# Kernel tuning notes

Hardware: AMD Instinct MI355X
Metric: run time of the kernel (lower is better)

## Reference

```python
import jax, jax.numpy as jnp
import numpy as np

T, N, F = 96, 1140, 64   # timesteps, nodes per graph, node feature dim
H = 32                    # GAT hidden channels
LH = 250                  # LSTM hidden
OUT = 2280                # per-head output
E = 22800                 # edges per graph


def setup_inputs() -> dict:
    key = jax.random.key(0)
    ks = jax.random.split(key, 32)
    s = lambda k, shape, fan: jax.random.normal(k, shape, jnp.float32) / np.sqrt(fan)
    inp = {}
    inp["nodes"] = jax.random.normal(ks[0], (T, N, F), jnp.float32)
    inp["edges_index"] = jax.random.randint(ks[1], (T, 2, E), 0, N)
    inp["edges_attr"] = jax.random.normal(ks[2], (T, E), jnp.float32)  # unused by forward (faithful)
    # GAT layer 1 (F -> H) and layer 2 (H -> H), heads=1
    inp["gat_W1"] = s(ks[3], (F, H), F)
    inp["gat_as1"] = s(ks[4], (H,), H)
    inp["gat_ad1"] = s(ks[5], (H,), H)
    inp["gat_b1"] = jnp.zeros((H,), jnp.float32)
    inp["gat_W2"] = s(ks[6], (H, H), H)
    inp["gat_as2"] = s(ks[7], (H,), H)
    inp["gat_ad2"] = s(ks[8], (H,), H)
    inp["gat_b2"] = jnp.zeros((H,), jnp.float32)
    # 2-layer LSTM, batch_first, batch=1, input = N*H
    IN0 = N * H
    inp["Wih0"] = s(ks[9], (4 * LH, IN0), IN0)
    inp["Whh0"] = s(ks[10], (4 * LH, LH), LH)
    inp["bih0"] = jnp.zeros((4 * LH,), jnp.float32)
    inp["bhh0"] = jnp.zeros((4 * LH,), jnp.float32)
    inp["Wih1"] = s(ks[11], (4 * LH, LH), LH)
    inp["Whh1"] = s(ks[12], (4 * LH, LH), LH)
    inp["bih1"] = jnp.zeros((4 * LH,), jnp.float32)
    inp["bhh1"] = jnp.zeros((4 * LH,), jnp.float32)
    # random initial states (original uses torch.randn in forward)
    inp["h0"] = jax.random.normal(ks[13], (2, 1, LH), jnp.float32)
    inp["c0"] = jax.random.normal(ks[14], (2, 1, LH), jnp.float32)
    for i in range(4):
        inp[f"fc{i+1}_W"] = s(ks[15 + 2 * i], (OUT, LH), LH)
        inp[f"fc{i+1}_b"] = jnp.zeros((OUT,), jnp.float32)
    return inp


def _gat_conv(x, src, dst, W, a_s, a_d, b, n):
    # GATConv, heads=1: h = xW; e_ij = LeakyReLU(a_s.h_src + a_d.h_dst);
    # softmax over edges sharing a destination; scatter-add aggregation.
    h = x @ W                                                   # [N, H]
    e = jax.nn.leaky_relu((h @ a_s)[src] + (h @ a_d)[dst], negative_slope=0.2)
    m = jax.ops.segment_max(e, dst, num_segments=n)
    ex = jnp.exp(e - m[dst])
    denom = jax.ops.segment_sum(ex, dst, num_segments=n)
    alpha = ex / denom[dst]
    return jax.ops.segment_sum(alpha[:, None] * h[src], dst, num_segments=n) + b


def _lstm_layer(xs, Wih, Whh, bih, bhh, h0, c0):
    # xs: [T, B, in]; torch gate order i, f, g, o
    def step(carry, x):
        h, c = carry
        g = x @ Wih.T + h @ Whh.T + bih + bhh
        i, f, gg, o = jnp.split(g, 4, axis=-1)
        c = jax.nn.sigmoid(f) * c + jax.nn.sigmoid(i) * jnp.tanh(gg)
        h = jax.nn.sigmoid(o) * jnp.tanh(c)
        return (h, c), h
    (_, _), ys = jax.lax.scan(step, (h0, c0), xs)
    return ys


def reference(nodes, edges_index, edges_attr, gat_W1, gat_as1, gat_ad1, gat_b1,
              gat_W2, gat_as2, gat_ad2, gat_b2,
              Wih0, Whh0, bih0, bhh0, Wih1, Whh1, bih1, bhh1, h0, c0,
              fc1_W, fc1_b, fc2_W, fc2_b, fc3_W, fc3_b, fc4_W, fc4_b):
    n = nodes.shape[1]
    loop = jnp.arange(n)  # self-loops (GATConv default add_self_loops=True)

    def per_graph(x, ei):
        src = jnp.concatenate([ei[0], loop])
        dst = jnp.concatenate([ei[1], loop])
        h = jax.nn.relu(_gat_conv(x, src, dst, gat_W1, gat_as1, gat_ad1, gat_b1, n))
        h = _gat_conv(h, src, dst, gat_W2, gat_as2, gat_ad2, gat_b2, n)
        return h.reshape(-1)

    seq = jax.vmap(per_graph)(nodes, edges_index)   # [T, N*H]
    xs = seq[:, None, :]                            # [T, 1, N*H] (batch=1)
    ys = _lstm_layer(xs, Wih0, Whh0, bih0, bhh0, h0[0], c0[0])
    ys = _lstm_layer(ys, Wih1, Whh1, bih1, bhh1, h0[1], c0[1])
    last = ys[-1]                                   # [1, LH]
    preds = [last @ fc1_W.T + fc1_b, last @ fc2_W.T + fc2_b,
             last @ fc3_W.T + fc3_b, last @ fc4_W.T + fc4_b]
    return jnp.stack(preds, axis=0).reshape(last.shape[0], 4, -1)  # [1, 4, 2280]
```

## Files before the change

### kernel.cpp

```cpp
#include <hip/hip_runtime.h>

#define T_ 96
#define N_ 1140
#define F_ 64
#define H_ 32
#define E_ 22800
#define LH_ 250
#define G4_ 1000
#define OUT_ 2280
#define KIN_ 36480
#define SPLITK 60
#define KC 32
#define BN 32
#define FEATB 13680
#define CNTB 8550

typedef _Float16 h2_t __attribute__((ext_vector_type(2)));

__device__ __forceinline__ float leaky02(float x){ return x > 0.f ? x : 0.2f*x; }
__device__ __forceinline__ float fsigm(float x){ return 1.f/(1.f + __expf(-x)); }
__device__ __forceinline__ float ftanh(float x){
  x = fminf(fmaxf(x, -15.f), 15.f);
  float t = __expf(2.f * x);
  return (t - 1.f) / (t + 1.f);
}
__device__ __forceinline__ unsigned packh2(float a, float b) {
  auto p = __builtin_amdgcn_cvt_pkrtz(a, b);
  return __builtin_bit_cast(unsigned, p);
}
__device__ __forceinline__ float fdot2u(unsigned w, unsigned h, float acc) {
  return __builtin_amdgcn_fdot2(__builtin_bit_cast(h2_t, w),
                                __builtin_bit_cast(h2_t, h), acc, false);
}

__device__ __forceinline__ void st_agent_u(unsigned* p, unsigned v) {
  __hip_atomic_store(p, v, __ATOMIC_RELAXED, __HIP_MEMORY_SCOPE_AGENT);
}
__device__ __forceinline__ unsigned ld_agent_u(const unsigned* p) {
  return __hip_atomic_load((unsigned*)p, __ATOMIC_RELAXED, __HIP_MEMORY_SCOPE_AGENT);
}
__device__ __forceinline__ void st_agent_i(int* p, int v) {
  __hip_atomic_store(p, v, __ATOMIC_RELAXED, __HIP_MEMORY_SCOPE_AGENT);
}
__device__ __forceinline__ int ld_agent_i(const int* p) {
  return __hip_atomic_load((int*)p, __ATOMIC_RELAXED, __HIP_MEMORY_SCOPE_AGENT);
}

__global__ void k_featcnt(const float* __restrict__ x, const float* __restrict__ W,
                          const float* __restrict__ as_, const float* __restrict__ ad_,
                          float* __restrict__ Hout, float* __restrict__ HS,
                          float* __restrict__ HD,
                          const int* __restrict__ ei, int* __restrict__ counts) {
  int tid = threadIdx.x;
  if (blockIdx.x >= FEATB) {
    int gid = (blockIdx.x - FEATB) * 256 + tid;
    if (gid >= T_ * E_) return;
    int t = gid / E_; int k = gid - t * E_;
    int dst = ei[(size_t)t * 2 * E_ + E_ + k];
    atomicAdd(&counts[t * N_ + dst], 1);
    return;
  }
  __shared__ float Wl[F_ * H_];
  __shared__ float asl[32], adl[32];
  for (int i = tid; i < F_ * H_; i += 256) Wl[i] = W[i];
  if (tid < 32) { asl[tid] = as_[tid]; adl[tid] = ad_[tid]; }
  __syncthreads();
  int row = blockIdx.x * 8 + (tid >> 5);
  int c = tid & 31;
  const float4* xr = (const float4*)(x + (size_t)row * F_);
  float acc = 0.f;
  for (int k4 = 0; k4 < (F_ >> 2); ++k4) {
    float4 v = xr[k4];
    acc += v.x * Wl[(4 * k4 + 0) * H_ + c];
    acc += v.y * Wl[(4 * k4 + 1) * H_ + c];
    acc += v.z * Wl[(4 * k4 + 2) * H_ + c];
    acc += v.w * Wl[(4 * k4 + 3) * H_ + c];
  }
  Hout[(size_t)row * H_ + c] = acc;
  float ps = acc * asl[c], pd = acc * adl[c];
  #pragma unroll
  for (int off = 16; off > 0; off >>= 1) {
    ps += __shfl_xor(ps, off, 32);
    pd += __shfl_xor(pd, off, 32);
  }
  if (c == 0) { HS[row] = ps; HD[row] = pd; }
}

__global__ void k_scan(const int* __restrict__ counts, int* __restrict__ offs,
                       int* __restrict__ cursor) {
  int t = blockIdx.x; int tid = threadIdx.x;
  int base = tid * 5;
  int v[5]; int s = 0;
  #pragma unroll
  for (int r = 0; r < 5; ++r) {
    int i = base + r;
    int c = (i < N_) ? counts[t * N_ + i] : 0;
    v[r] = c; s += c;
  }
  __shared__ int sh[256];
  sh[tid] = s; __syncthreads();
  for (int off = 1; off < 256; off <<= 1) {
    int add = (tid >= off) ? sh[tid - off] : 0;
    __syncthreads();
    sh[tid] += add;
    __syncthreads();
  }
  int run = sh[tid] - s;
  #pragma unroll
  for (int r = 0; r < 5; ++r) {
    int i = base + r;
    if (i < N_) { offs[t * (N_ + 1) + i] = run; cursor[t * N_ + i] = run; }
    run += v[r];
  }
  if (tid == 255) offs[t * (N_ + 1) + N_] = sh[255];
}

__global__ void k_fill(const int* __restrict__ ei, int* __restrict__ cursor,
                       int* __restrict__ elist) {
  int gid = blockIdx.x * blockDim.x + threadIdx.x;
  if (gid >= T_ * E_) return;
  int t = gid / E_; int k = gid - t * E_;
  int src = ei[(size_t)t * 2 * E_ + k];
  int dst = ei[(size_t)t * 2 * E_ + E_ + k];
  int pos = atomicAdd(&cursor[t * N_ + dst], 1);
  elist[(size_t)t * E_ + pos] = src;
}

__global__ void k_aggrfeat(const float* __restrict__ Hf, const float* __restrict__ HS,
                           const float* __restrict__ HD, const int* __restrict__ offs,
                           const int* __restrict__ elist, const float* __restrict__ b,
                           const float* __restrict__ W2, const float* __restrict__ as2,
                           const float* __restrict__ ad2,
                           float* __restrict__ H2, float* __restrict__ HS2,
                           float* __restrict__ HD2) {
  __shared__ float W2l[H_ * H_];
  __shared__ float as2l[32], ad2l[32];
  int tid = threadIdx.x;
  for (int i = tid; i < H_ * H_; i += 256) W2l[i] = W2[i];
  if (tid < 32) { as2l[tid] = as2[tid]; ad2l[tid] = ad2[tid]; }
  __syncthreads();
  int gid = blockIdx.x * 256 + tid;
  int row = gid >> 5; int c = gid & 31;
  if (row >= T_ * N_) return;
  int t = row / N_; int i = row - t * N_;
  float hd_i = HD[row];
  float m = leaky02(HS[row] + hd_i);
  float s = 1.f;
  float acc = Hf[(size_t)row * H_ + c];
  int e0 = offs[t * (N_ + 1) + i], e1 = offs[t * (N_ + 1) + i + 1];
  const int* el = elist + (size_t)t * E_;
  const float* Ht = Hf + (size_t)t * N_ * H_;
  const float* HSt = HS + t * N_;
  float hsA = 0.f, hvA = 0.f;
  if (e0 < e1) {
    int srcA = el[e0];
    hsA = HSt[srcA];
    hvA = Ht[(size_t)srcA * H_ + c];
  }
  for (int e = e0; e < e1; ++e) {
    float hs = hsA, hv = hvA;
    if (e + 1 < e1) {
      int srcA = el[e + 1];
      hsA = HSt[srcA];
      hvA = Ht[(size_t)srcA * H_ + c];
    }
    float eg = leaky02(hs + hd_i);
    float mn = fmaxf(m, eg);
    float scl = __expf(m - mn);
    float p = __expf(eg - mn);
    s = s * scl + p;
    acc = acc * scl + p * hv;
    m = mn;
  }
  float val = fmaxf(acc / s + b[c], 0.f);
  float acc2 = 0.f;
  #pragma unroll
  for (int cc = 0; cc < 32; ++cc) {
    float xc = __shfl(val, cc, 32);
    acc2 += xc * W2l[cc * H_ + c];
  }
  H2[(size_t)row * H_ + c] = acc2;
  float ps = acc2 * as2l[c], pd = acc2 * ad2l[c];
  #pragma unroll
  for (int off = 16; off > 0; off >>= 1) {
    ps += __shfl_xor(ps, off, 32);
    pd += __shfl_xor(pd, off, 32);
  }
  if (c == 0) { HS2[row] = ps; HD2[row] = pd; }
}

__global__ void k_aggr(const float* __restrict__ Hf, const float* __restrict__ HS,
                       const float* __restrict__ HD, const int* __restrict__ offs,
                       const int* __restrict__ elist, const float* __restrict__ b,
                       float* __restrict__ Xout) {
  int gid = blockIdx.x * blockDim.x + threadIdx.x;
  int row = gid >> 5; int c = gid & 31;
  if (row >= T_ * N_) return;
  int t = row / N_; int i = row - t * N_;
  float hd_i = HD[row];
  float m = leaky02(HS[row] + hd_i);
  float s = 1.f;
  float acc = Hf[(size_t)row * H_ + c];
  int e0 = offs[t * (N_ + 1) + i], e1 = offs[t * (N_ + 1) + i + 1];
  const int* el = elist + (size_t)t * E_;
  const float* Ht = Hf + (size_t)t * N_ * H_;
  const float* HSt = HS + t * N_;
  float hsA = 0.f, hvA = 0.f;
  if (e0 < e1) {
    int srcA = el[e0];
    hsA = HSt[srcA];
    hvA = Ht[(size_t)srcA * H_ + c];
  }
  for (int e = e0; e < e1; ++e) {
    float hs = hsA, hv = hvA;
    if (e + 1 < e1) {
      int srcA = el[e + 1];
      hsA = HSt[srcA];
      hvA = Ht[(size_t)srcA * H_ + c];
    }
    float eg = leaky02(hs + hd_i);
    float mn = fmaxf(m, eg);
    float scl = __expf(m - mn);
    float p = __expf(eg - mn);
    s = s * scl + p;
    acc = acc * scl + p * hv;
    m = mn;
  }
  Xout[(size_t)row * H_ + c] = acc / s + b[c];
}

__global__ void k_gemm(const float* __restrict__ X, const float* __restrict__ Wih,
                       float* __restrict__ Gpart) {
  __shared__ unsigned Xs[T_][KC / 2 + 1];
  __shared__ unsigned Ws[BN][KC / 2 + 1];
  int j0 = blockIdx.x * BN;
  int sp = blockIdx.y;
  int tid = threadIdx.x;
  int jj = tid & 7;
  int tt = tid >> 3;
  float acc[6][4] = {};
  int kbeg = sp * (KIN_ / SPLITK);
  int kend = kbeg + (KIN_ / SPLITK);
  for (int k0 = kbeg; k0 < kend; k0 += KC) {
    for (int idx = tid; idx < T_ * (KC / 2); idx += 128) {
      int tr = idx >> 4; int kk = idx & 15;
      const float2 v = *(const float2*)(X + (size_t)tr * KIN_ + k0 + 2 * kk);
      Xs[tr][kk] = packh2(v.x, v.y);
    }
    for (int idx = tid; idx < BN * (KC / 2); idx += 128) {
      int jr = idx >> 4; int kk = idx & 15;
      int j = j0 + jr;
      unsigned v = 0;
      if (j < G4_) {
        const float2 w = *(const float2*)(Wih + (size_t)j * KIN_ + k0 + 2 * kk);
        v = packh2(w.x, w.y);
      }
      Ws[jr][kk] = v;
    }
    __syncthreads();
    for (int kk = 0; kk < KC / 2; ++kk) {
      unsigned xv[6], wv[4];
      #pragma unroll
      for (int r = 0; r < 6; ++r) xv[r] = Xs[tt * 6 + r][kk];
      #pragma unroll
      for (int q = 0; q < 4; ++q) wv[q] = Ws[jj * 4 + q][kk];
      #pragma unroll
      for (int r = 0; r < 6; ++r)
        #pragma unroll
        for (int q = 0; q < 4; ++q)
          acc[r][q] = fdot2u(wv[q], xv[r], acc[r][q]);
    }
    __syncthreads();
  }
  #pragma unroll
  for (int r = 0; r < 6; ++r) {
    int t = tt * 6 + r;
    #pragma unroll
    for (int q = 0; q < 4; ++q) {
      int j = j0 + jj * 4 + q;
      if (j < G4_) Gpart[((size_t)sp * T_ + t) * 1024 + j] = acc[r][q];
    }
  }
}

__global__ void k_gred(const float* __restrict__ Gpart, const float* __restrict__ bih,
                       const float* __restrict__ bhh, float* __restrict__ G0) {
  int idx = blockIdx.x * blockDim.x + threadIdx.x;
  if (idx >= T_ * G4_) return;
  int t = idx / G4_; int jg = idx - t * G4_;
  int j = jg >> 2, g = jg & 3;
  int c = g * LH_ + j;
  float s = bih[c] + bhh[c];
  for (int sp = 0; sp < SPLITK; ++sp) s += Gpart[((size_t)sp * T_ + t) * 1024 + c];
  G0[idx] = s;
}

__global__ void __launch_bounds__(512, 2) k_lstm(
    const float* __restrict__ G0, const float* __restrict__ Whh0,
    const float* __restrict__ Wih1, const float* __restrict__ Whh1,
    const float* __restrict__ bih1, const float* __restrict__ bhh1,
    const float* __restrict__ h0in, const float* __restrict__ c0in,
    unsigned* __restrict__ hp,
    int* __restrict__ flags,
    float* __restrict__ ylast) {
  int tid = threadIdx.x;
  int bid = blockIdx.x;
  int wv = bid * 8 + (tid >> 6);
  int lane = tid & 63;
  int qg = lane >> 4;
  int ql = lane & 15;

  unsigned w0[4][8], wx1[4][8], wh1[4][8];
  float bs1[4], c0l[4], c1l[4];
  bool act[4];
  #pragma unroll
  for (int u = 0; u < 4; ++u) {
    int U = wv * 4 + u;
    act[u] = (U < LH_);
    int Uc = act[u] ? U : 0;
    size_t rb = (size_t)(qg * LH_ + Uc) * LH_;
    #pragma unroll
    for (int m = 0; m < 8; ++m) {
      int pi = m * 16 + ql;
      if (act[u] && pi < 125) {
        w0[u][m]  = packh2(Whh0[rb + 2 * pi], Whh0[rb + 2 * pi + 1]);
        wx1[u][m] = packh2(Wih1[rb + 2 * pi], Wih1[rb + 2 * pi + 1]);
        wh1[u][m] = packh2(Whh1[rb + 2 * pi], Whh1[rb + 2 * pi + 1]);
      } else { w0[u][m] = 0; wx1[u][m] = 0; wh1[u][m] = 0; }
    }
    bs1[u] = act[u] ? (bih1[qg * LH_ + Uc] + bhh1[qg * LH_ + Uc]) : 0.f;
    c0l[u] = act[u] ? c0in[Uc] : 0.f;
    c1l[u] = act[u] ? c0in[LH_ + Uc] : 0.f;
  }

  float gpre[4];
  #pragma unroll
  for (int u = 0; u < 4; ++u)
    gpre[u] = act[u] ? G0[0 * G4_ + (wv * 4 + u) * 4 + qg] : 0.f;

  for (int p = 0; p <= T_; ++p) {
    int rs = (p - 1) & 1, wslot = p & 1;
    unsigned x0p[8], h1p[8];
    if (p == 0) {
      #pragma unroll
      for (int m = 0; m < 8; ++m) {
        int pi = m * 16 + ql;
        x0p[m] = (pi < 125) ? packh2(h0in[2 * pi], h0in[2 * pi + 1]) : 0u;
      }
    } else {
      #pragma unroll
      for (int m = 0; m < 8; ++m)
        x0p[m] = ld_agent_u(&hp[rs * 256 + m * 16 + ql]);
      if (p == 1) {
        #pragma unroll
        for (int m = 0; m < 8; ++m) {
          int pi = m * 16 + ql;
          h1p[m] = (pi < 125) ? packh2(h0in[LH_ + 2 * pi], h0in[LH_ + 2 * pi + 1]) : 0u;
        }
      } else {
        #pragma unroll
        for (int m = 0; m < 8; ++m)
          h1p[m] = ld_agent_u(&hp[rs * 256 + 128 + m * 16 + ql]);
      }
    }

    if (p < T_) {
      float h0new[4];
      #pragma unroll
      for (int u = 0; u < 4; ++u) {
        float s = 0.f;
        #pragma unroll
        for (int m = 0; m < 8; ++m) s = fdot2u(w0[u][m], x0p[m], s);
        s += __shfl_xor(s, 1); s += __shfl_xor(s, 2);
        s += __shfl_xor(s, 4); s += __shfl_xor(s, 8);
        float pre = s + gpre[u];
        float a = (qg == 2) ? ftanh(pre) : fsigm(pre);
        float ai = __shfl(a, ql);
        float af = __shfl(a, 16 + ql);
        float ag = __shfl(a, 32 + ql);
        float ao = __shfl(a, 48 + ql);
        c0l[u] = af * c0l[u] + ai * ag;
        h0new[u] = act[u] ? (ao * ftanh(c0l[u])) : 0.f;
      }
      if (lane == 0) {
        st_agent_u(&hp[wslot * 256 + 2 * wv],     packh2(h0new[0], h0new[1]));
        st_agent_u(&hp[wslot * 256 + 2 * wv + 1], packh2(h0new[2], h0new[3]));
      }
    }
    if (p >= 1) {
      float h1new[4];
      #pragma unroll
      for (int u = 0; u < 4; ++u) {
        float s = 0.f;
        #pragma unroll
        for (int m = 0; m < 8; ++m) s = fdot2u(wx1[u][m], x0p[m], s);
        #pragma unroll
        for (int m = 0; m < 8; ++m) s = fdot2u(wh1[u][m], h1p[m], s);
        s += __shfl_xor(s, 1); s += __shfl_xor(s, 2);
        s += __shfl_xor(s, 4); s += __shfl_xor(s, 8);
        float pre = s + bs1[u];
        float a = (qg == 2) ? ftanh(pre) : fsigm(pre);
        float bi = __shfl(a, ql);
        float bf = __shfl(a, 16 + ql);
        float bg = __shfl(a, 32 + ql);
        float bo = __shfl(a, 48 + ql);
        c1l[u] = bf * c1l[u] + bi * bg;
        h1new[u] = act[u] ? (bo * ftanh(c1l[u])) : 0.f;
      }
      if (p - 1 == T_ - 1 && lane == 0) {
        #pragma unroll
        for (int u = 0; u < 4; ++u)
          if (act[u]) ylast[wv * 4 + u] = h1new[u];
      }
      if (lane == 0) {
        st_agent_u(&hp[wslot * 256 + 128 + 2 * wv],     packh2(h1new[0], h1new[1]));
        st_agent_u(&hp[wslot * 256 + 128 + 2 * wv + 1], packh2(h1new[2], h1new[3]));
      }
    }
    float gnext[4];
    #pragma unroll
    for (int u = 0; u < 4; ++u)
      gnext[u] = (p + 1 < T_ && act[u]) ? G0[(p + 1) * G4_ + (wv * 4 + u) * 4 + qg] : 0.f;
    if (p < T_) {
      __syncthreads();
      if (tid == 0) {
        asm volatile("s_waitcnt vmcnt(0)" ::: "memory");
        st_agent_i(&flags[bid], p + 1);
      }
      if (tid < 64) {
        int guard = 0;
        for (;;) {
          int f = ld_agent_i(&flags[lane & 7]);
          if (__ballot(f >= p + 1) == ~0ULL) break;
          if (++guard > (1 << 22)) break;
          __builtin_amdgcn_s_sleep(1);
        }
      }
      __syncthreads();
    }
    #pragma unroll
    for (int u = 0; u < 4; ++u) gpre[u] = gnext[u];
  }
}

__global__ void k_fc(const float* __restrict__ ylast,
                     const float* __restrict__ Wa, const float* __restrict__ ba,
                     const float* __restrict__ Wb, const float* __restrict__ bb,
                     const float* __restrict__ Wc, const float* __restrict__ bc,
                     const float* __restrict__ Wd, const float* __restrict__ bd,
                     float* __restrict__ out) {
  int wg = blockIdx.x * 4 + (threadIdx.x >> 6);
  int lane = threadIdx.x & 63;
  if (wg >= 4 * OUT_) return;
  int head = wg / OUT_, o = wg - head * OUT_;
  const float* W = head == 0 ? Wa : head == 1 ? Wb : head == 2 ? Wc : Wd;
  const float* b = head == 0 ? ba : head == 1 ? bb : head == 2 ? bc : bd;
  float s = 0.f;
  #pragma unroll
  for (int r = 0; r < 4; ++r) {
    int idx = r * 64 + lane;
    if (idx < LH_) s += ylast[idx] * W[(size_t)o * LH_ + idx];
  }
  #pragma unroll
  for (int off = 32; off > 0; off >>= 1) s += __shfl_xor(s, off, 64);
  if (lane == 0) out[wg] = s + b[o];
}

extern "C" void kernel_launch(void* const* d_in, const int* in_sizes, int n_in,
                              void* d_out, int out_size, void* d_ws, size_t ws_size,
                              hipStream_t stream) {
  const float* nodes = (const float*)d_in[0];
  const int*   ei    = (const int*)d_in[1];
  const float* W1    = (const float*)d_in[3];
  const float* as1   = (const float*)d_in[4];
  const float* ad1   = (const float*)d_in[5];
  const float* b1    = (const float*)d_in[6];
  const float* W2    = (const float*)d_in[7];
  const float* as2   = (const float*)d_in[8];
  const float* ad2   = (const float*)d_in[9];
  const float* b2    = (const float*)d_in[10];
  const float* Wih0  = (const float*)d_in[11];
  const float* Whh0  = (const float*)d_in[12];
  const float* bih0  = (const float*)d_in[13];
  const float* bhh0  = (const float*)d_in[14];
  const float* Wih1  = (const float*)d_in[15];
  const float* Whh1  = (const float*)d_in[16];
  const float* bih1  = (const float*)d_in[17];
  const float* bhh1  = (const float*)d_in[18];
  const float* h0    = (const float*)d_in[19];
  const float* c0    = (const float*)d_in[20];
  const float* fW1   = (const float*)d_in[21];
  const float* fb1   = (const float*)d_in[22];
  const float* fW2   = (const float*)d_in[23];
  const float* fb2   = (const float*)d_in[24];
  const float* fW3   = (const float*)d_in[25];
  const float* fb3   = (const float*)d_in[26];
  const float* fW4   = (const float*)d_in[27];
  const float* fb4   = (const float*)d_in[28];
  float* out = (float*)d_out;

  const size_t o_Gpart  = 0;
  const size_t o_H      = 0;
  const size_t o_HS     = 14008320;
  const size_t o_HD     = 14446080;
  const size_t o_H2     = 14883840;
  const size_t o_X2     = 28892160;
  const size_t o_flags  = 42900480;
  const size_t o_counts = 42900736;
  const size_t o_offs   = 43338496;
  const size_t o_cursor = 43776640;
  const size_t o_elist  = 44214400;
  const size_t o_G0     = 52969600;
  const size_t o_hp     = 53353600;
  const size_t o_ylast  = 53355648;
  const size_t o_HS2    = 53356672;
  const size_t o_HD2    = 53794432;
  const size_t total    = 54232192;
  if (ws_size < total) return;

  char* ws = (char*)d_ws;
  float*    Gpart  = (float*)(ws + o_Gpart);
  float*    Hbuf   = (float*)(ws + o_H);
  float*    HS     = (float*)(ws + o_HS);
  float*    HD     = (float*)(ws + o_HD);
  float*    H2     = (float*)(ws + o_H2);
  float*    X2     = (float*)(ws + o_X2);
  int*      flags  = (int*)(ws + o_flags);
  int*      counts = (int*)(ws + o_counts);
  int*      offs   = (int*)(ws + o_offs);
  int*      cursor = (int*)(ws + o_cursor);
  int*      elist  = (int*)(ws + o_elist);
  float*    G0     = (float*)(ws + o_G0);
  unsigned* hp     = (unsigned*)(ws + o_hp);
  float*    ylast  = (float*)(ws + o_ylast);
  float*    HS2    = (float*)(ws + o_HS2);
  float*    HD2    = (float*)(ws + o_HD2);

  (void)hipMemsetAsync(ws + o_flags, 0, 256 + (size_t)T_ * N_ * 4, stream);

  const int rows_grid = (T_ * N_ * H_) / 256;

  k_featcnt<<<FEATB + CNTB, 256, 0, stream>>>(nodes, W1, as1, ad1,
                                              Hbuf, HS, HD, ei, counts);
  k_scan<<<T_, 256, 0, stream>>>(counts, offs, cursor);
  k_fill<<<CNTB, 256, 0, stream>>>(ei, cursor, elist);
  k_aggrfeat<<<rows_grid, 256, 0, stream>>>(Hbuf, HS, HD, offs, elist, b1,
                                            W2, as2, ad2, H2, HS2, HD2);
  k_aggr<<<rows_grid, 256, 0, stream>>>(H2, HS2, HD2, offs, elist, b2, X2);
  k_gemm<<<dim3(32, SPLITK), 128, 0, stream>>>(X2, Wih0, Gpart);
  k_gred<<<(T_ * G4_ + 255) / 256, 256, 0, stream>>>(Gpart, bih0, bhh0, G0);
  k_lstm<<<8, 512, 0, stream>>>(G0, Whh0, Wih1, Whh1, bih1, bhh1, h0, c0,
                                hp, flags, ylast);
  k_fc<<<OUT_, 256, 0, stream>>>(ylast, fW1, fb1, fW2, fb2, fW3, fb3, fW4, fb4, out);
}
```

Before: 1.086 ms.

## Build per-graph CSR in shared memory inside feature kernel; deepen gather prefetch

The count, scan and fill kernels are merged into the first feature kernel. Each of T extra blocks builds its graph's CSR using shared-memory counters and cursors, which removes two launches, the global counts and cursor buffers, and most of the memset. The aggregation loops now prefetch two edges ahead instead of one to hide gather latency. The risk is that the CSR work is serialized into only 96 blocks of 256 threads, which could become a tail at the end of the feature kernel, and that all feature blocks now reserve the larger shared-memory footprint, which can lower occupancy.

```diff
diff --git a/kernel.cpp b/kernel.cpp
--- a/kernel.cpp
+++ b/kernel.cpp
@@ -13,7 +13,6 @@
 #define KC 32
 #define BN 32
 #define FEATB 13680
-#define CNTB 8550
 
 typedef _Float16 h2_t __attribute__((ext_vector_type(2)));
 
@@ -46,22 +45,56 @@
   return __hip_atomic_load((int*)p, __ATOMIC_RELAXED, __HIP_MEMORY_SCOPE_AGENT);
 }
 
-__global__ void k_featcnt(const float* __restrict__ x, const float* __restrict__ W,
+__global__ void k_featcsr(const float* __restrict__ x, const float* __restrict__ W,
                           const float* __restrict__ as_, const float* __restrict__ ad_,
                           float* __restrict__ Hout, float* __restrict__ HS,
                           float* __restrict__ HD,
-                          const int* __restrict__ ei, int* __restrict__ counts) {
+                          const int* __restrict__ ei, int* __restrict__ offs,
+                          int* __restrict__ elist) {
+  __shared__ float Wl[F_ * H_];
+  __shared__ float asl[32], adl[32];
+  __shared__ int cnt[N_], cur[N_], sh[256];
   int tid = threadIdx.x;
   if (blockIdx.x >= FEATB) {
-    int gid = (blockIdx.x - FEATB) * 256 + tid;
-    if (gid >= T_ * E_) return;
-    int t = gid / E_; int k = gid - t * E_;
-    int dst = ei[(size_t)t * 2 * E_ + E_ + k];
-    atomicAdd(&counts[t * N_ + dst], 1);
+    int t = blockIdx.x - FEATB;
+    const int* srcp = ei + (size_t)t * 2 * E_;
+    const int* dstp = srcp + E_;
+    for (int i = tid; i < N_; i += 256) cnt[i] = 0;
+    __syncthreads();
+    for (int k = tid; k < E_; k += 256) atomicAdd(&cnt[dstp[k]], 1);
+    __syncthreads();
+    int base = tid * 5;
+    int v[5]; int s = 0;
+    #pragma unroll
+    for (int r = 0; r < 5; ++r) {
+      int i = base + r;
+      int c = (i < N_) ? cnt[i] : 0;
+      v[r] = c; s += c;
+    }
+    sh[tid] = s; __syncthreads();
+    for (int off = 1; off < 256; off <<= 1) {
+      int add = (tid >= off) ? sh[tid - off] : 0;
+      __syncthreads();
+      sh[tid] += add;
+      __syncthreads();
+    }
+    int run = sh[tid] - s;
+    #pragma unroll
+    for (int r = 0; r < 5; ++r) {
+      int i = base + r;
+      if (i < N_) { offs[t * (N_ + 1) + i] = run; cur[i] = run; }
+      run += v[r];
+    }
+    if (tid == 255) offs[t * (N_ + 1) + N_] = sh[255];
+    __syncthreads();
+    int* elt = elist + (size_t)t * E_;
+    for (int k = tid; k < E_; k += 256) {
+      int src = srcp[k];
+      int pos = atomicAdd(&cur[dstp[k]], 1);
+      elt[pos] = src;
+    }
     return;
   }
-  __shared__ float Wl[F_ * H_];
-  __shared__ float asl[32], adl[32];
   for (int i = tid; i < F_ * H_; i += 256) Wl[i] = W[i];
   if (tid < 32) { asl[tid] = as_[tid]; adl[tid] = ad_[tid]; }
   __syncthreads();
@@ -84,46 +117,6 @@
     pd += __shfl_xor(pd, off, 32);
   }
   if (c == 0) { HS[row] = ps; HD[row] = pd; }
-}
-
-__global__ void k_scan(const int* __restrict__ counts, int* __restrict__ offs,
-                       int* __restrict__ cursor) {
-  int t = blockIdx.x; int tid = threadIdx.x;
-  int base = tid * 5;
-  int v[5]; int s = 0;
-  #pragma unroll
-  for (int r = 0; r < 5; ++r) {
-    int i = base + r;
-    int c = (i < N_) ? counts[t * N_ + i] : 0;
-    v[r] = c; s += c;
-  }
-  __shared__ int sh[256];
-  sh[tid] = s; __syncthreads();
-  for (int off = 1; off < 256; off <<= 1) {
-    int add = (tid >= off) ? sh[tid - off] : 0;
-    __syncthreads();
-    sh[tid] += add;
-    __syncthreads();
-  }
-  int run = sh[tid] - s;
-  #pragma unroll
-  for (int r = 0; r < 5; ++r) {
-    int i = base + r;
-    if (i < N_) { offs[t * (N_ + 1) + i] = run; cursor[t * N_ + i] = run; }
-    run += v[r];
-  }
-  if (tid == 255) offs[t * (N_ + 1) + N_] = sh[255];
-}
-
-__global__ void k_fill(const int* __restrict__ ei, int* __restrict__ cursor,
-                       int* __restrict__ elist) {
-  int gid = blockIdx.x * blockDim.x + threadIdx.x;
-  if (gid >= T_ * E_) return;
-  int t = gid / E_; int k = gid - t * E_;
-  int src = ei[(size_t)t * 2 * E_ + k];
-  int dst = ei[(size_t)t * 2 * E_ + E_ + k];
-  int pos = atomicAdd(&cursor[t * N_ + dst], 1);
-  elist[(size_t)t * E_ + pos] = src;
 }
 
 __global__ void k_aggrfeat(const float* __restrict__ Hf, const float* __restrict__ HS,
@@ -151,18 +144,18 @@
   const int* el = elist + (size_t)t * E_;
   const float* Ht = Hf + (size_t)t * N_ * H_;
   const float* HSt = HS + t * N_;
-  float hsA = 0.f, hvA = 0.f;
+  float hsA = 0.f, hvA = 0.f, hsB = 0.f, hvB = 0.f;
   if (e0 < e1) {
-    int srcA = el[e0];
-    hsA = HSt[srcA];
-    hvA = Ht[(size_t)srcA * H_ + c];
+    int sA = el[e0]; hsA = HSt[sA]; hvA = Ht[(size_t)sA * H_ + c];
+  }
+  if (e0 + 1 < e1) {
+    int sB = el[e0 + 1]; hsB = HSt[sB]; hvB = Ht[(size_t)sB * H_ + c];
   }
   for (int e = e0; e < e1; ++e) {
     float hs = hsA, hv = hvA;
-    if (e + 1 < e1) {
-      int srcA = el[e + 1];
-      hsA = HSt[srcA];
-      hvA = Ht[(size_t)srcA * H_ + c];
+    hsA = hsB; hvA = hvB;
+    if (e + 2 < e1) {
+      int sB = el[e + 2]; hsB = HSt[sB]; hvB = Ht[(size_t)sB * H_ + c];
     }
     float eg = leaky02(hs + hd_i);
     float mn = fmaxf(m, eg);
@@ -205,18 +198,18 @@
   const int* el = elist + (size_t)t * E_;
   const float* Ht = Hf + (size_t)t * N_ * H_;
   const float* HSt = HS + t * N_;
-  float hsA = 0.f, hvA = 0.f;
+  float hsA = 0.f, hvA = 0.f, hsB = 0.f, hvB = 0.f;
   if (e0 < e1) {
-    int srcA = el[e0];
-    hsA = HSt[srcA];
-    hvA = Ht[(size_t)srcA * H_ + c];
+    int sA = el[e0]; hsA = HSt[sA]; hvA = Ht[(size_t)sA * H_ + c];
+  }
+  if (e0 + 1 < e1) {
+    int sB = el[e0 + 1]; hsB = HSt[sB]; hvB = Ht[(size_t)sB * H_ + c];
   }
   for (int e = e0; e < e1; ++e) {
     float hs = hsA, hv = hvA;
-    if (e + 1 < e1) {
-      int srcA = el[e + 1];
-      hsA = HSt[srcA];
-      hvA = Ht[(size_t)srcA * H_ + c];
+    hsA = hsB; hvA = hvB;
+    if (e + 2 < e1) {
+      int sB = el[e + 2]; hsB = HSt[sB]; hvB = Ht[(size_t)sB * H_ + c];
     }
     float eg = leaky02(hs + hd_i);
     float mn = fmaxf(m, eg);
@@ -506,16 +499,14 @@
   const size_t o_H2     = 14883840;
   const size_t o_X2     = 28892160;
   const size_t o_flags  = 42900480;
-  const size_t o_counts = 42900736;
-  const size_t o_offs   = 43338496;
-  const size_t o_cursor = 43776640;
-  const size_t o_elist  = 44214400;
-  const size_t o_G0     = 52969600;
-  const size_t o_hp     = 53353600;
-  const size_t o_ylast  = 53355648;
-  const size_t o_HS2    = 53356672;
-  const size_t o_HD2    = 53794432;
-  const size_t total    = 54232192;
+  const size_t o_offs   = 42900736;
+  const size_t o_elist  = 43338880;
+  const size_t o_G0     = 52094080;
+  const size_t o_hp     = 52478080;
+  const size_t o_ylast  = 52480128;
+  const size_t o_HS2    = 52481152;
+  const size_t o_HD2    = 52918912;
+  const size_t total    = 53356672;
   if (ws_size < total) return;
 
   char* ws = (char*)d_ws;
@@ -526,9 +517,7 @@
   float*    H2     = (float*)(ws + o_H2);
   float*    X2     = (float*)(ws + o_X2);
   int*      flags  = (int*)(ws + o_flags);
-  int*      counts = (int*)(ws + o_counts);
   int*      offs   = (int*)(ws + o_offs);
-  int*      cursor = (int*)(ws + o_cursor);
   int*      elist  = (int*)(ws + o_elist);
   float*    G0     = (float*)(ws + o_G0);
   unsigned* hp     = (unsigned*)(ws + o_hp);
@@ -536,14 +525,12 @@
   float*    HS2    = (float*)(ws + o_HS2);
   float*    HD2    = (float*)(ws + o_HD2);
 
-  (void)hipMemsetAsync(ws + o_flags, 0, 256 + (size_t)T_ * N_ * 4, stream);
+  (void)hipMemsetAsync(flags, 0, 256, stream);
 
   const int rows_grid = (T_ * N_ * H_) / 256;
 
-  k_featcnt<<<FEATB + CNTB, 256, 0, stream>>>(nodes, W1, as1, ad1,
-                                              Hbuf, HS, HD, ei, counts);
-  k_scan<<<T_, 256, 0, stream>>>(counts, offs, cursor);
-  k_fill<<<CNTB, 256, 0, stream>>>(ei, cursor, elist);
+  k_featcsr<<<FEATB + T_, 256, 0, stream>>>(nodes, W1, as1, ad1,
+                                            Hbuf, HS, HD, ei, offs, elist);
   k_aggrfeat<<<rows_grid, 256, 0, stream>>>(Hbuf, HS, HD, offs, elist, b1,
                                             W2, as2, ad2, H2, HS2, HD2);
   k_aggr<<<rows_grid, 256, 0, stream>>>(H2, HS2, HD2, offs, elist, b2, X2);
```

After: 1.033 ms. 1.05x faster.
